# Optimization experiments

Measured on AMD Instinct MI355X. Metric: run time of the kernel, lower is better.

Reference implementation:

```python
import jax, jax.numpy as jnp
import numpy as np

SEQ, EMBED, VOCAB = 2048, 128, 50257

def setup_inputs() -> dict:
    key = jax.random.key(0)
    ks = jax.random.split(key, 6)
    return {
        "psi_real": jax.random.normal(ks[0], (SEQ, EMBED), dtype=jnp.float32),
        "psi_imag": jax.random.normal(ks[1], (SEQ, EMBED), dtype=jnp.float32),
        # original: torch.randn(vocab, embed, complex64) * 0.1
        "patterns_real": jax.random.normal(ks[2], (VOCAB, EMBED), dtype=jnp.float32) * 0.1,
        "patterns_imag": jax.random.normal(ks[3], (VOCAB, EMBED), dtype=jnp.float32) * 0.1,
        # nn.Linear(embed, vocab): W [vocab, embed], b [vocab]
        "W": jax.random.normal(ks[4], (VOCAB, EMBED), dtype=jnp.float32) * (1.0 / np.sqrt(EMBED)),
        "b": jax.random.normal(ks[5], (VOCAB,), dtype=jnp.float32) * 0.01,
    }

def reference(psi_real, psi_imag, patterns_real, patterns_imag, W, b):
    psi = jax.lax.complex(psi_real, psi_imag)            # [S, E] complex
    patterns = jax.lax.complex(patterns_real, patterns_imag)  # [V, E] complex
    # torch.vdot(psi[i], pattern_j) = sum(conj(psi[i]) * pattern_j)
    # -> batched: conj(psi) @ patterns.T, then |.|^2
    scores = jnp.einsum('se,ve->sv', jnp.conj(psi), patterns)  # [S, V] complex
    interference_logits = (scores.real ** 2 + scores.imag ** 2).astype(jnp.float32)
    linear_logits = psi_real @ W.T + b                    # Linear on psi.real
    return interference_logits + linear_logits
```

## Files before the change

### kernel.cpp

```cpp
#include <hip/hip_runtime.h>

static constexpr int S  = 2048;
static constexpr int E  = 128;
static constexpr int V  = 50257;

typedef __attribute__((ext_vector_type(8))) short bf16x8;
typedef __attribute__((ext_vector_type(4))) float floatx4;

#define MF(a, b, c) __builtin_amdgcn_mfma_f32_16x16x32_bf16((a), (b), (c), 0, 0, 0)

static constexpr int  RT       = S / 16;
static constexpr int  NBLK     = (V + 63) / 64;
static constexpr int  CT       = NBLK * 4;
static constexpr long A_MAT    = (long)RT * 4 * 64 * 8;
static constexpr long B_MAT    = (long)CT * 4 * 64 * 8;
static constexpr long WS_SHORTS = 4 * A_MAT + 6 * B_MAT;
static constexpr long WS_BYTES  = WS_SHORTS * 2;

__device__ __forceinline__ void split2(float x, unsigned short& hi, unsigned short& lo) {
    unsigned xb = __float_as_uint(x);
    hi = (unsigned short)(xb >> 16);
    float hf = __uint_as_float(xb & 0xFFFF0000u);
    lo = (unsigned short)(__float_as_uint(x - hf) >> 16);
}

__device__ __forceinline__ void cvt8(const float* v, bf16x8& hi, bf16x8& lo) {
    #pragma unroll
    for (int j = 0; j < 8; j++) {
        unsigned short h, l;
        split2(v[j], h, l);
        hi[j] = (short)h;
        lo[j] = (short)l;
    }
}

__global__ __launch_bounds__(256)
void pre_a(const float* __restrict__ psi_r, const float* __restrict__ psi_i,
           short* __restrict__ ws)
{
    const int t    = blockIdx.x * 256 + threadIdx.x;
    const int lane = t & 63;
    const int kc   = (t >> 6) & 3;
    const int rt   = t >> 8;
    const int row  = rt * 16 + (lane & 15);
    const int k0   = kc * 32 + (lane >> 4) * 8;

    float v[8];
    const float* p = psi_r + (long)row * E + k0;
    #pragma unroll
    for (int j = 0; j < 8; j++) v[j] = p[j];
    bf16x8 hi, lo; cvt8(v, hi, lo);
    *(bf16x8*)(ws + 0 * A_MAT + (long)t * 8) = hi;
    *(bf16x8*)(ws + 1 * A_MAT + (long)t * 8) = lo;

    p = psi_i + (long)row * E + k0;
    #pragma unroll
    for (int j = 0; j < 8; j++) v[j] = p[j];
    cvt8(v, hi, lo);
    *(bf16x8*)(ws + 2 * A_MAT + (long)t * 8) = hi;
    *(bf16x8*)(ws + 3 * A_MAT + (long)t * 8) = lo;
}

__global__ __launch_bounds__(256)
void pre_b(const float* __restrict__ pat_r, const float* __restrict__ pat_i,
           const float* __restrict__ Wm, short* __restrict__ ws)
{
    const int t    = blockIdx.x * 256 + threadIdx.x;
    const int lane = t & 63;
    const int kc   = (t >> 6) & 3;
    const int ct   = t >> 8;
    const int row  = ct * 16 + (lane & 15);
    const int k0   = kc * 32 + (lane >> 4) * 8;
    const bool ok  = row < V;

    short* B0 = ws + 4 * A_MAT;
    const float* srcs[3] = { pat_r, pat_i, Wm };
    #pragma unroll
    for (int s = 0; s < 3; s++) {
        float v[8];
        if (ok) {
            const float* p = srcs[s] + (long)row * E + k0;
            #pragma unroll
            for (int j = 0; j < 8; j++) v[j] = p[j];
        } else {
            #pragma unroll
            for (int j = 0; j < 8; j++) v[j] = 0.f;
        }
        bf16x8 hi, lo; cvt8(v, hi, lo);
        *(bf16x8*)(B0 + (long)(2 * s)     * B_MAT + (long)t * 8) = hi;
        *(bf16x8*)(B0 + (long)(2 * s + 1) * B_MAT + (long)t * 8) = lo;
    }
}

__global__ __launch_bounds__(256, 2)
void interference_mfma(const short* __restrict__ ws,
                       const float* __restrict__ bias,
                       float* __restrict__ out)
{
    const int tid  = threadIdx.x;
    const int wave = tid >> 6;
    const int lane = tid & 63;
    const int quad = lane >> 4;
    const int r16  = lane & 15;
    const int wm   = wave >> 1;
    const int wn   = wave & 1;
    const int mb   = blockIdx.x;
    const int nb   = blockIdx.y;

    const short* Ah = ws + 0 * A_MAT;
    const short* Al = ws + 1 * A_MAT;
    const short* Ih = ws + 2 * A_MAT;
    const short* Il = ws + 3 * A_MAT;
    const short* Bm = ws + 4 * A_MAT;

    const int rt0 = mb * 8 + wm * 4;
    const int ct0 = nb * 4 + wn * 2;

    floatx4 Cr[4][2], Ci[4][2], Cl[4][2];
    #pragma unroll
    for (int mi = 0; mi < 4; mi++)
        #pragma unroll
        for (int ni = 0; ni < 2; ni++) {
            Cr[mi][ni] = floatx4{0.f, 0.f, 0.f, 0.f};
            Ci[mi][ni] = floatx4{0.f, 0.f, 0.f, 0.f};
            Cl[mi][ni] = floatx4{0.f, 0.f, 0.f, 0.f};
        }

    for (int kc = 0; kc < 4; kc++) {
        bf16x8 fB[6][2];
        #pragma unroll
        for (int m = 0; m < 6; m++)
            #pragma unroll
            for (int ni = 0; ni < 2; ni++)
                fB[m][ni] = *(const bf16x8*)(Bm + (long)m * B_MAT +
                                             (((long)(ct0 + ni) * 4 + kc) * 64 + lane) * 8);
        #pragma unroll
        for (int mi = 0; mi < 4; mi++) {
            const long ao = (((long)(rt0 + mi) * 4 + kc) * 64 + lane) * 8;
            bf16x8 ah = *(const bf16x8*)(Ah + ao);
            bf16x8 al = *(const bf16x8*)(Al + ao);
            bf16x8 ih = *(const bf16x8*)(Ih + ao);
            bf16x8 il = *(const bf16x8*)(Il + ao);
            #pragma unroll
            for (int ni = 0; ni < 2; ni++) {
                Cr[mi][ni] = MF(ah, fB[0][ni], Cr[mi][ni]);
                Cr[mi][ni] = MF(ah, fB[1][ni], Cr[mi][ni]);
                Cr[mi][ni] = MF(al, fB[0][ni], Cr[mi][ni]);
                Cr[mi][ni] = MF(ih, fB[2][ni], Cr[mi][ni]);
                Cr[mi][ni] = MF(ih, fB[3][ni], Cr[mi][ni]);
                Cr[mi][ni] = MF(il, fB[2][ni], Cr[mi][ni]);
                Ci[mi][ni] = MF(ah, fB[2][ni], Ci[mi][ni]);
                Ci[mi][ni] = MF(ah, fB[3][ni], Ci[mi][ni]);
                Ci[mi][ni] = MF(al, fB[2][ni], Ci[mi][ni]);
                Cl[mi][ni] = MF(ah, fB[4][ni], Cl[mi][ni]);
                Cl[mi][ni] = MF(ah, fB[5][ni], Cl[mi][ni]);
                Cl[mi][ni] = MF(al, fB[4][ni], Cl[mi][ni]);
            }
            ih = ih ^ (short)0x8000;
            il = il ^ (short)0x8000;
            #pragma unroll
            for (int ni = 0; ni < 2; ni++) {
                Ci[mi][ni] = MF(ih, fB[0][ni], Ci[mi][ni]);
                Ci[mi][ni] = MF(ih, fB[1][ni], Ci[mi][ni]);
                Ci[mi][ni] = MF(il, fB[0][ni], Ci[mi][ni]);
            }
        }
    }

    #pragma unroll
    for (int ni = 0; ni < 2; ni++) {
        const int col = nb * 64 + wn * 32 + ni * 16 + r16;
        if (col < V) {
            const float bv = bias[col];
            #pragma unroll
            for (int mi = 0; mi < 4; mi++) {
                const int rbase = mb * 128 + wm * 64 + mi * 16 + quad * 4;
                #pragma unroll
                for (int r = 0; r < 4; r++) {
                    float cr = Cr[mi][ni][r];
                    float ci = Ci[mi][ni][r];
                    float cl = Cl[mi][ni][r];
                    out[(long)(rbase + r) * V + col] = cr * cr + ci * ci + cl + bv;
                }
            }
        }
    }
}

static constexpr int MB = 128;
static constexpr int NB = 48;
static constexpr int KP = 40;

__global__ __launch_bounds__(256, 2)
void interference_kernel(const float* __restrict__ psi_r,
                         const float* __restrict__ psi_i,
                         const float* __restrict__ pat_r,
                         const float* __restrict__ pat_i,
                         const float* __restrict__ Wm,
                         const float* __restrict__ bias,
                         float* __restrict__ out)
{
    __shared__ short smem[4 * MB * KP + 6 * NB * KP];
    short* sA = smem;
    short* sB = smem + 4 * MB * KP;

    const int tid  = threadIdx.x;
    const int wave = tid >> 6;
    const int lane = tid & 63;
    const int quad = lane >> 4;
    const int r16  = lane & 15;

    const int m0 = blockIdx.y * MB;
    const int v0 = blockIdx.x * NB;

    floatx4 Cr[2][3], Ci[2][3], Cl[2][3];
    #pragma unroll
    for (int mi = 0; mi < 2; mi++)
        #pragma unroll
        for (int ni = 0; ni < 3; ni++) {
            Cr[mi][ni] = floatx4{0.f, 0.f, 0.f, 0.f};
            Ci[mi][ni] = floatx4{0.f, 0.f, 0.f, 0.f};
            Cl[mi][ni] = floatx4{0.f, 0.f, 0.f, 0.f};
        }

    for (int chunk = 0; chunk < E / 32; chunk++) {
        const int kc = chunk * 32;
        #pragma unroll
        for (int i = 0; i < 8; i++) {
            int idx = tid + i * 256;
            int src = idx >> 10;
            int rem = idx & 1023;
            int row = rem >> 3;
            int kq  = rem & 7;
            const float* bsrc = src ? psi_i : psi_r;
            const float4 x = *(const float4*)(bsrc + (m0 + row) * E + kc + kq * 4);
            unsigned short h0, h1, h2, h3, l0, l1, l2, l3;
            split2(x.x, h0, l0); split2(x.y, h1, l1);
            split2(x.z, h2, l2); split2(x.w, h3, l3);
            int offh = ((src * 2) * MB + row) * KP + kq * 4;
            int offl = offh + MB * KP;
            uint2 uh = make_uint2((unsigned)h0 | ((unsigned)h1 << 16),
                                  (unsigned)h2 | ((unsigned)h3 << 16));
            uint2 ul = make_uint2((unsigned)l0 | ((unsigned)l1 << 16),
                                  (unsigned)l2 | ((unsigned)l3 << 16));
            *(uint2*)(sA + offh) = uh;
            *(uint2*)(sA + offl) = ul;
        }
        #pragma unroll
        for (int i = 0; i < 5; i++) {
            int idx = tid + i * 256;
            if (idx < 1152) {
                int src = idx / 384;
                int rem = idx - src * 384;
                int row = rem >> 3;
                int kq  = rem & 7;
                int vv  = v0 + row; if (vv > V - 1) vv = V - 1;
                const float* bsrc = (src == 0) ? pat_r : ((src == 1) ? pat_i : Wm);
                const float4 x = *(const float4*)(bsrc + vv * E + kc + kq * 4);
                unsigned short h0, h1, h2, h3, l0, l1, l2, l3;
                split2(x.x, h0, l0); split2(x.y, h1, l1);
                split2(x.z, h2, l2); split2(x.w, h3, l3);
                int offh = ((src * 2) * NB + row) * KP + kq * 4;
                int offl = offh + NB * KP;
                uint2 uh = make_uint2((unsigned)h0 | ((unsigned)h1 << 16),
                                      (unsigned)h2 | ((unsigned)h3 << 16));
                uint2 ul = make_uint2((unsigned)l0 | ((unsigned)l1 << 16),
                                      (unsigned)l2 | ((unsigned)l3 << 16));
                *(uint2*)(sB + offh) = uh;
                *(uint2*)(sB + offl) = ul;
            }
        }
        __syncthreads();

        bf16x8 fB[6][3];
        #pragma unroll
        for (int bm = 0; bm < 6; bm++)
            #pragma unroll
            for (int ni = 0; ni < 3; ni++)
                fB[bm][ni] = *(const bf16x8*)(sB + (bm * NB + ni * 16 + r16) * KP + quad * 8);

        #pragma unroll
        for (int mi = 0; mi < 2; mi++) {
            const int ab = (wave * 32 + mi * 16 + r16) * KP + quad * 8;
            bf16x8 Prh = *(const bf16x8*)(sA + ab);
            bf16x8 Prl = *(const bf16x8*)(sA + ab + MB * KP);
            bf16x8 Pih = *(const bf16x8*)(sA + ab + 2 * MB * KP);
            bf16x8 Pil = *(const bf16x8*)(sA + ab + 3 * MB * KP);
            #pragma unroll
            for (int ni = 0; ni < 3; ni++) {
                Cr[mi][ni] = MF(Prh, fB[0][ni], Cr[mi][ni]);
                Cr[mi][ni] = MF(Prh, fB[1][ni], Cr[mi][ni]);
                Cr[mi][ni] = MF(Prl, fB[0][ni], Cr[mi][ni]);
                Cr[mi][ni] = MF(Pih, fB[2][ni], Cr[mi][ni]);
                Cr[mi][ni] = MF(Pih, fB[3][ni], Cr[mi][ni]);
                Cr[mi][ni] = MF(Pil, fB[2][ni], Cr[mi][ni]);
                Ci[mi][ni] = MF(Prh, fB[2][ni], Ci[mi][ni]);
                Ci[mi][ni] = MF(Prh, fB[3][ni], Ci[mi][ni]);
                Ci[mi][ni] = MF(Prl, fB[2][ni], Ci[mi][ni]);
                Cl[mi][ni] = MF(Prh, fB[4][ni], Cl[mi][ni]);
                Cl[mi][ni] = MF(Prh, fB[5][ni], Cl[mi][ni]);
                Cl[mi][ni] = MF(Prl, fB[4][ni], Cl[mi][ni]);
            }
            Pih = Pih ^ (short)0x8000;
            Pil = Pil ^ (short)0x8000;
            #pragma unroll
            for (int ni = 0; ni < 3; ni++) {
                Ci[mi][ni] = MF(Pih, fB[0][ni], Ci[mi][ni]);
                Ci[mi][ni] = MF(Pih, fB[1][ni], Ci[mi][ni]);
                Ci[mi][ni] = MF(Pil, fB[0][ni], Ci[mi][ni]);
            }
        }
        __syncthreads();
    }

    #pragma unroll
    for (int ni = 0; ni < 3; ni++) {
        const int col = v0 + ni * 16 + r16;
        if (col < V) {
            const float bv = bias[col];
            #pragma unroll
            for (int mi = 0; mi < 2; mi++) {
                const int rbase = m0 + wave * 32 + mi * 16 + quad * 4;
                #pragma unroll
                for (int r = 0; r < 4; r++) {
                    float cr = Cr[mi][ni][r];
                    float ci = Ci[mi][ni][r];
                    float cl = Cl[mi][ni][r];
                    out[(long)(rbase + r) * V + col] = cr * cr + ci * ci + cl + bv;
                }
            }
        }
    }
}

extern "C" void kernel_launch(void* const* d_in, const int* in_sizes, int n_in,
                              void* d_out, int out_size, void* d_ws, size_t ws_size,
                              hipStream_t stream) {
    const float* psi_r = (const float*)d_in[0];
    const float* psi_i = (const float*)d_in[1];
    const float* pat_r = (const float*)d_in[2];
    const float* pat_i = (const float*)d_in[3];
    const float* Wm    = (const float*)d_in[4];
    const float* b     = (const float*)d_in[5];
    float* out = (float*)d_out;

    if (d_ws && ws_size >= (size_t)WS_BYTES) {
        short* ws = (short*)d_ws;
        pre_a<<<RT * 4 * 64 / 256, 256, 0, stream>>>(psi_r, psi_i, ws);
        pre_b<<<CT * 4 * 64 / 256, 256, 0, stream>>>(pat_r, pat_i, Wm, ws);
        interference_mfma<<<dim3(S / 128, NBLK), 256, 0, stream>>>(ws, b, out);
    } else {
        dim3 grid((V + NB - 1) / NB, S / MB);
        interference_kernel<<<grid, dim3(256), 0, stream>>>(psi_r, psi_i, pat_r, pat_i, Wm, b, out);
    }
}
```

Before: 804.0 us.

## Merge preprocessing kernels and double-buffer MFMA operand loads across k-chunks

```diff
diff --git a/kernel.cpp b/kernel.cpp
--- a/kernel.cpp
+++ b/kernel.cpp
@@ -35,62 +35,120 @@
 }
 
 __global__ __launch_bounds__(256)
-void pre_a(const float* __restrict__ psi_r, const float* __restrict__ psi_i,
-           short* __restrict__ ws)
+void pre_all(const float* __restrict__ psi_r, const float* __restrict__ psi_i,
+             const float* __restrict__ pat_r, const float* __restrict__ pat_i,
+             const float* __restrict__ Wm, short* __restrict__ ws)
 {
-    const int t    = blockIdx.x * 256 + threadIdx.x;
-    const int lane = t & 63;
-    const int kc   = (t >> 6) & 3;
-    const int rt   = t >> 8;
-    const int row  = rt * 16 + (lane & 15);
-    const int k0   = kc * 32 + (lane >> 4) * 8;
-
-    float v[8];
-    const float* p = psi_r + (long)row * E + k0;
-    #pragma unroll
-    for (int j = 0; j < 8; j++) v[j] = p[j];
-    bf16x8 hi, lo; cvt8(v, hi, lo);
-    *(bf16x8*)(ws + 0 * A_MAT + (long)t * 8) = hi;
-    *(bf16x8*)(ws + 1 * A_MAT + (long)t * 8) = lo;
-
-    p = psi_i + (long)row * E + k0;
-    #pragma unroll
-    for (int j = 0; j < 8; j++) v[j] = p[j];
-    cvt8(v, hi, lo);
-    *(bf16x8*)(ws + 2 * A_MAT + (long)t * 8) = hi;
-    *(bf16x8*)(ws + 3 * A_MAT + (long)t * 8) = lo;
-}
-
-__global__ __launch_bounds__(256)
-void pre_b(const float* __restrict__ pat_r, const float* __restrict__ pat_i,
-           const float* __restrict__ Wm, short* __restrict__ ws)
-{
-    const int t    = blockIdx.x * 256 + threadIdx.x;
-    const int lane = t & 63;
-    const int kc   = (t >> 6) & 3;
-    const int ct   = t >> 8;
-    const int row  = ct * 16 + (lane & 15);
-    const int k0   = kc * 32 + (lane >> 4) * 8;
-    const bool ok  = row < V;
-
-    short* B0 = ws + 4 * A_MAT;
-    const float* srcs[3] = { pat_r, pat_i, Wm };
-    #pragma unroll
-    for (int s = 0; s < 3; s++) {
+    if (blockIdx.x < 128) {
+        const int t    = blockIdx.x * 256 + threadIdx.x;
+        const int lane = t & 63;
+        const int kc   = (t >> 6) & 3;
+        const int rt   = t >> 8;
+        const int row  = rt * 16 + (lane & 15);
+        const int k0   = kc * 32 + (lane >> 4) * 8;
+
         float v[8];
-        if (ok) {
-            const float* p = srcs[s] + (long)row * E + k0;
-            #pragma unroll
-            for (int j = 0; j < 8; j++) v[j] = p[j];
-        } else {
-            #pragma unroll
-            for (int j = 0; j < 8; j++) v[j] = 0.f;
-        }
+        const float* p = psi_r + (long)row * E + k0;
+        #pragma unroll
+        for (int j = 0; j < 8; j++) v[j] = p[j];
         bf16x8 hi, lo; cvt8(v, hi, lo);
-        *(bf16x8*)(B0 + (long)(2 * s)     * B_MAT + (long)t * 8) = hi;
-        *(bf16x8*)(B0 + (long)(2 * s + 1) * B_MAT + (long)t * 8) = lo;
-    }
-}
+        *(bf16x8*)(ws + 0 * A_MAT + (long)t * 8) = hi;
+        *(bf16x8*)(ws + 1 * A_MAT + (long)t * 8) = lo;
+
+        p = psi_i + (long)row * E + k0;
+        #pragma unroll
+        for (int j = 0; j < 8; j++) v[j] = p[j];
+        cvt8(v, hi, lo);
+        *(bf16x8*)(ws + 2 * A_MAT + (long)t * 8) = hi;
+        *(bf16x8*)(ws + 3 * A_MAT + (long)t * 8) = lo;
+    } else {
+        const int t    = (blockIdx.x - 128) * 256 + threadIdx.x;
+        const int lane = t & 63;
+        const int kc   = (t >> 6) & 3;
+        const int ct   = t >> 8;
+        const int row  = ct * 16 + (lane & 15);
+        const int k0   = kc * 32 + (lane >> 4) * 8;
+        const bool ok  = row < V;
+
+        short* B0 = ws + 4 * A_MAT;
+        const float* srcs[3] = { pat_r, pat_i, Wm };
+        #pragma unroll
+        for (int s = 0; s < 3; s++) {
+            float v[8];
+            if (ok) {
+                const float* p = srcs[s] + (long)row * E + k0;
+                #pragma unroll
+                for (int j = 0; j < 8; j++) v[j] = p[j];
+            } else {
+                #pragma unroll
+                for (int j = 0; j < 8; j++) v[j] = 0.f;
+            }
+            bf16x8 hi, lo; cvt8(v, hi, lo);
+            *(bf16x8*)(B0 + (long)(2 * s)     * B_MAT + (long)t * 8) = hi;
+            *(bf16x8*)(B0 + (long)(2 * s + 1) * B_MAT + (long)t * 8) = lo;
+        }
+    }
+}
+
+
+#define PREF_A(dst, mi_, kc_) do {                                              \
+    const int ao_ = (((rt0 + (mi_)) * 4 + (kc_)) * 64 + lane) * 8;              \
+    dst[0] = *(const bf16x8*)(Ah + ao_);                                        \
+    dst[1] = *(const bf16x8*)(Al + ao_);                                        \
+    dst[2] = *(const bf16x8*)(Ih + ao_);                                        \
+    dst[3] = *(const bf16x8*)(Il + ao_);                                        \
+} while (0)
+
+#define PREF_B3(dst, m0_, kc_) do {                                             \
+    _Pragma("unroll")                                                           \
+    for (int m_ = (m0_); m_ < (m0_) + 3; m_++) {                                \
+        _Pragma("unroll")                                                       \
+        for (int ni_ = 0; ni_ < 2; ni_++)                                       \
+            dst[m_][ni_] = *(const bf16x8*)(Bm + (long)m_ * B_MAT +             \
+                (long)((((ct0 + ni_) * 4 + (kc_)) * 64 + lane) * 8));           \
+    }                                                                           \
+} while (0)
+
+#define MFMA_STEP(A_, B_, mi_) do {                                             \
+    _Pragma("unroll")                                                           \
+    for (int ni_ = 0; ni_ < 2; ni_++) {                                         \
+        Cr[mi_][ni_] = MF(A_[0], B_[0][ni_], Cr[mi_][ni_]);                     \
+        Cr[mi_][ni_] = MF(A_[0], B_[1][ni_], Cr[mi_][ni_]);                     \
+        Cr[mi_][ni_] = MF(A_[1], B_[0][ni_], Cr[mi_][ni_]);                     \
+        Cr[mi_][ni_] = MF(A_[2], B_[2][ni_], Cr[mi_][ni_]);                     \
+        Cr[mi_][ni_] = MF(A_[2], B_[3][ni_], Cr[mi_][ni_]);                     \
+        Cr[mi_][ni_] = MF(A_[3], B_[2][ni_], Cr[mi_][ni_]);                     \
+        Ci[mi_][ni_] = MF(A_[0], B_[2][ni_], Ci[mi_][ni_]);                     \
+        Ci[mi_][ni_] = MF(A_[0], B_[3][ni_], Ci[mi_][ni_]);                     \
+        Ci[mi_][ni_] = MF(A_[1], B_[2][ni_], Ci[mi_][ni_]);                     \
+        Cl[mi_][ni_] = MF(A_[0], B_[4][ni_], Cl[mi_][ni_]);                     \
+        Cl[mi_][ni_] = MF(A_[0], B_[5][ni_], Cl[mi_][ni_]);                     \
+        Cl[mi_][ni_] = MF(A_[1], B_[4][ni_], Cl[mi_][ni_]);                     \
+    }                                                                           \
+    {                                                                           \
+        bf16x8 ihn_ = A_[2] ^ (short)0x8000;                                    \
+        bf16x8 iln_ = A_[3] ^ (short)0x8000;                                    \
+        _Pragma("unroll")                                                       \
+        for (int ni_ = 0; ni_ < 2; ni_++) {                                     \
+            Ci[mi_][ni_] = MF(ihn_, B_[0][ni_], Ci[mi_][ni_]);                  \
+            Ci[mi_][ni_] = MF(ihn_, B_[1][ni_], Ci[mi_][ni_]);                  \
+            Ci[mi_][ni_] = MF(iln_, B_[0][ni_], Ci[mi_][ni_]);                  \
+        }                                                                       \
+    }                                                                           \
+} while (0)
+
+#define KC_STEP(kc_, CURB, NXTB, LAST)  do {                                    \
+    PREF_A(fAb, 1, kc_);                                                        \
+    if (!(LAST)) PREF_B3(NXTB, 0, (kc_) + 1);                                   \
+    MFMA_STEP(fAa, CURB, 0);                                                    \
+    PREF_A(fAa, 2, kc_);                                                        \
+    if (!(LAST)) PREF_B3(NXTB, 3, (kc_) + 1);                                   \
+    MFMA_STEP(fAb, CURB, 1);                                                    \
+    PREF_A(fAb, 3, kc_);                                                        \
+    MFMA_STEP(fAa, CURB, 2);                                                    \
+    if (!(LAST)) PREF_A(fAa, 0, (kc_) + 1);                                     \
+    MFMA_STEP(fAb, CURB, 3);                                                    \
+} while (0)
 
 __global__ __launch_bounds__(256, 2)
 void interference_mfma(const short* __restrict__ ws,
@@ -126,46 +184,17 @@
             Cl[mi][ni] = floatx4{0.f, 0.f, 0.f, 0.f};
         }
 
-    for (int kc = 0; kc < 4; kc++) {
-        bf16x8 fB[6][2];
-        #pragma unroll
-        for (int m = 0; m < 6; m++)
-            #pragma unroll
-            for (int ni = 0; ni < 2; ni++)
-                fB[m][ni] = *(const bf16x8*)(Bm + (long)m * B_MAT +
-                                             (((long)(ct0 + ni) * 4 + kc) * 64 + lane) * 8);
-        #pragma unroll
-        for (int mi = 0; mi < 4; mi++) {
-            const long ao = (((long)(rt0 + mi) * 4 + kc) * 64 + lane) * 8;
-            bf16x8 ah = *(const bf16x8*)(Ah + ao);
-            bf16x8 al = *(const bf16x8*)(Al + ao);
-            bf16x8 ih = *(const bf16x8*)(Ih + ao);
-            bf16x8 il = *(const bf16x8*)(Il + ao);
-            #pragma unroll
-            for (int ni = 0; ni < 2; ni++) {
-                Cr[mi][ni] = MF(ah, fB[0][ni], Cr[mi][ni]);
-                Cr[mi][ni] = MF(ah, fB[1][ni], Cr[mi][ni]);
-                Cr[mi][ni] = MF(al, fB[0][ni], Cr[mi][ni]);
-                Cr[mi][ni] = MF(ih, fB[2][ni], Cr[mi][ni]);
-                Cr[mi][ni] = MF(ih, fB[3][ni], Cr[mi][ni]);
-                Cr[mi][ni] = MF(il, fB[2][ni], Cr[mi][ni]);
-                Ci[mi][ni] = MF(ah, fB[2][ni], Ci[mi][ni]);
-                Ci[mi][ni] = MF(ah, fB[3][ni], Ci[mi][ni]);
-                Ci[mi][ni] = MF(al, fB[2][ni], Ci[mi][ni]);
-                Cl[mi][ni] = MF(ah, fB[4][ni], Cl[mi][ni]);
-                Cl[mi][ni] = MF(ah, fB[5][ni], Cl[mi][ni]);
-                Cl[mi][ni] = MF(al, fB[4][ni], Cl[mi][ni]);
-            }
-            ih = ih ^ (short)0x8000;
-            il = il ^ (short)0x8000;
-            #pragma unroll
-            for (int ni = 0; ni < 2; ni++) {
-                Ci[mi][ni] = MF(ih, fB[0][ni], Ci[mi][ni]);
-                Ci[mi][ni] = MF(ih, fB[1][ni], Ci[mi][ni]);
-                Ci[mi][ni] = MF(il, fB[0][ni], Ci[mi][ni]);
-            }
-        }
-    }
+    bf16x8 fBa[6][2], fBb[6][2];
+    bf16x8 fAa[4],    fAb[4];
+
+    PREF_B3(fBa, 0, 0);
+    PREF_B3(fBa, 3, 0);
+    PREF_A(fAa, 0, 0);
+
+    KC_STEP(0, fBa, fBb, 0);
+    KC_STEP(1, fBb, fBa, 0);
+    KC_STEP(2, fBa, fBb, 0);
+    KC_STEP(3, fBb, fBa, 1);
 
     #pragma unroll
     for (int ni = 0; ni < 2; ni++) {
@@ -346,8 +375,7 @@
 
     if (d_ws && ws_size >= (size_t)WS_BYTES) {
         short* ws = (short*)d_ws;
-        pre_a<<<RT * 4 * 64 / 256, 256, 0, stream>>>(psi_r, psi_i, ws);
-        pre_b<<<CT * 4 * 64 / 256, 256, 0, stream>>>(pat_r, pat_i, Wm, ws);
+        pre_all<<<128 + CT * 4 * 64 / 256, 256, 0, stream>>>(psi_r, psi_i, pat_r, pat_i, Wm, ws);
         interference_mfma<<<dim3(S / 128, NBLK), 256, 0, stream>>>(ws, b, out);
     } else {
         dim3 grid((V + NB - 1) / NB, S / MB);
```

Result: no change. 814.0 us (+1.2%).
